# Kernel optimization log

Hardware: AMD Instinct MI355X
Metric: run time of the kernel (lower is better)

## Reference

```python
import jax, jax.numpy as jnp
import numpy as np
import math

N_QUBITS = 6
N_LAYERS = 3
OUT_DIM = 8
B = 131072
F = 24


def _gate_rx(a):
    # RX(a) = [[cos(a/2), -i sin(a/2)], [-i sin(a/2), cos(a/2)]]; a: scalar or [B]
    c = jnp.cos(a / 2).astype(jnp.complex64)
    s = (-1j * jnp.sin(a / 2)).astype(jnp.complex64)
    return jnp.stack([jnp.stack([c, s], -1), jnp.stack([s, c], -1)], -2)


def _gate_ry(a):
    c = jnp.cos(a / 2).astype(jnp.complex64)
    s = jnp.sin(a / 2).astype(jnp.complex64)
    return jnp.stack([jnp.stack([c, -s], -1), jnp.stack([s, c], -1)], -2)


def _gate_rz(a):
    # RZ(a) = diag(e^{-ia/2}, e^{ia/2})
    e = jnp.exp(-0.5j * a.astype(jnp.complex64))
    z = jnp.zeros_like(e)
    return jnp.stack([jnp.stack([e, z], -1), jnp.stack([z, jnp.conj(e)], -1)], -2)


def _apply_1q(state, gate, q, batched):
    # state: [B] + [2]*N_QUBITS ; gate: [2,2] or [B,2,2]
    s = jnp.moveaxis(state, 1 + q, 1)
    if batched:
        out = jnp.einsum('bij,bj...->bi...', gate, s)
    else:
        out = jnp.einsum('ij,bj...->bi...', gate, s)
    return jnp.moveaxis(out, 1, 1 + q)


def _apply_cnot(state, c, t):
    # flip target where control bit == 1
    cax = 1 + c
    s0 = jnp.take(state, 0, axis=cax)
    s1 = jnp.take(state, 1, axis=cax)
    tax = 1 + t if t < c else t  # control axis removed
    s1 = jnp.flip(s1, axis=tax)
    return jnp.stack([s0, s1], axis=cax)


def _circuit(x, theta):
    Bn = x.shape[0]
    # pooling branch of forward: chunks of size ceil(F/n_qubits)=4, mean each
    x_packed = x.reshape(Bn, N_QUBITS, F // N_QUBITS).mean(-1)
    angles = jnp.clip(x_packed, -6.0, 6.0) / 6.0 * math.pi  # [B, n_qubits]

    state = jnp.zeros((Bn,) + (2,) * N_QUBITS, dtype=jnp.complex64)
    state = state.at[(slice(None),) + (0,) * N_QUBITS].set(1.0)

    # angle encoding: RX(a_q), RZ(0.5*a_q) per qubit (batched gates)
    for q in range(N_QUBITS):
        state = _apply_1q(state, _gate_rx(angles[:, q]), q, batched=True)
        state = _apply_1q(state, _gate_rz(0.5 * angles[:, q]), q, batched=True)

    for l in range(N_LAYERS):
        for q in range(N_QUBITS - 1):
            state = _apply_cnot(state, q, q + 1)
        state = _apply_cnot(state, N_QUBITS - 1, 0)
        for q in range(N_QUBITS):
            state = _apply_1q(state, _gate_rx(theta[l, q, 0]), q, batched=False)
            state = _apply_1q(state, _gate_ry(theta[l, q, 1]), q, batched=False)
            state = _apply_1q(state, _gate_rz(theta[l, q, 2]), q, batched=False)

    probs = jnp.abs(state) ** 2  # real
    meas = []
    for k in range(OUT_DIM):
        q = k % N_QUBITS
        if k % 2 == 0:  # PauliZ
            pq = jnp.sum(probs, axis=tuple(a for a in range(1, N_QUBITS + 1) if a != 1 + q))
            meas.append(pq[:, 0] - pq[:, 1])
        else:  # PauliX: Re <psi| X_q |psi>
            flipped = jnp.flip(state, axis=1 + q)
            meas.append(jnp.real(jnp.sum(jnp.conj(state) * flipped, axis=tuple(range(1, N_QUBITS + 1)))))
    return jnp.stack(meas, axis=1).astype(jnp.float32)  # [B, out_dim]


def setup_inputs() -> dict:
    key = jax.random.key(0)
    k1, k2 = jax.random.split(key)
    x = jax.random.normal(k1, (B, F), dtype=jnp.float32)
    theta = jax.random.normal(k2, (N_LAYERS, N_QUBITS, 3), dtype=jnp.float32) * 0.1
    return {"x": x, "theta": theta}


def reference(x, theta):
    return _circuit(x, theta)
```

## Files before the change

kernel.cpp:

```cpp
#include <hip/hip_runtime.h>
#include <math.h>


typedef _Float16 half8v __attribute__((ext_vector_type(8)));
typedef _Float16 half4v __attribute__((ext_vector_type(4)));
typedef float    float4v __attribute__((ext_vector_type(4)));

__device__ __forceinline__ float2 pk_cmul(float2 g, float2 a) {
    float2 t;
    asm("v_pk_mul_f32 %0, %1, %2 op_sel:[0,0] op_sel_hi:[0,1]"
        : "=v"(t) : "v"(g), "v"(a));
    asm("v_pk_fma_f32 %0, %1, %2, %0 op_sel:[1,1,0] op_sel_hi:[1,0,1] neg_lo:[1,0,0]"
        : "+v"(t) : "v"(g), "v"(a));
    return t;
}
__device__ __forceinline__ float2 pk_cmac(float2 acc, float2 g, float2 a) {
    asm("v_pk_fma_f32 %0, %1, %2, %0 op_sel:[0,0,0] op_sel_hi:[0,1,1]"
        : "+v"(acc) : "v"(g), "v"(a));
    asm("v_pk_fma_f32 %0, %1, %2, %0 op_sel:[1,1,0] op_sel_hi:[1,0,1] neg_lo:[1,0,0]"
        : "+v"(acc) : "v"(g), "v"(a));
    return acc;
}

__device__ __forceinline__ float xpair(float v) {
    return __int_as_float(__builtin_amdgcn_mov_dpp(__float_as_int(v), 0xB1, 0xF, 0xF, true));
}
__device__ __forceinline__ float2 xpair2(float2 v) {
    return make_float2(xpair(v.x), xpair(v.y));
}

template<int M>
__device__ __forceinline__ void apply1q(float2* st, float2 g00, float2 g01,
                                        float2 g10, float2 g11) {
#pragma unroll
    for (int j = 0; j < 32; ++j) {
        if (j & M) continue;
        float2 a = st[j], b = st[j + M];
        float2 na = pk_cmul(g00, a); na = pk_cmac(na, g01, b);
        float2 nb = pk_cmul(g10, a); nb = pk_cmac(nb, g11, b);
        st[j] = na; st[j + M] = nb;
    }
}

template<int MC, int MT>
__device__ __forceinline__ void cnot(float2* st) {
#pragma unroll
    for (int j = 0; j < 32; ++j) {
        if ((j & MC) && !(j & MT)) {
            float2 tmp = st[j]; st[j] = st[j + MT]; st[j + MT] = tmp;
        }
    }
}

struct cf { float r, i; };
__device__ __forceinline__ cf scmul(cf a, cf b) {
    return { fmaf(a.r, b.r, -a.i * b.i), fmaf(a.r, b.i, a.i * b.r) };
}

__device__ __forceinline__ int rpos(int row, int k) {
    return ((((row >> 4) * 4 + (k >> 5)) * 4 + ((k >> 3) & 3)) * 16 + (row & 15)) * 8 + (k & 7);
}

__global__ __launch_bounds__(128) void ubuild_kernel(
    const float* __restrict__ theta, float* __restrict__ Rw) {
    __shared__ float2 gs[18 * 4];
    const int t = threadIdx.x;
    if (t < 18) {
        const float* th = theta + t * 3;
        float sx, cx, sy, cy, sz, cz;
        __sincosf(0.5f * th[0], &sx, &cx);
        __sincosf(0.5f * th[1], &sy, &cy);
        __sincosf(0.5f * th[2], &sz, &cz);
        cf m00 = {  cy * cx,  sy * sx };
        cf m01 = { -sy * cx, -cy * sx };
        cf m10 = {  sy * cx, -cy * sx };
        cf m11 = {  cy * cx, -sy * sx };
        cf e0 = { cz, -sz }, e1 = { cz, sz };
        cf g00 = scmul(e0, m00), g01 = scmul(e0, m01);
        cf g10 = scmul(e1, m10), g11 = scmul(e1, m11);
        float2* o = gs + t * 4;
        o[0] = make_float2(g00.r, g00.i);
        o[1] = make_float2(g01.r, g01.i);
        o[2] = make_float2(g10.r, g10.i);
        o[3] = make_float2(g11.r, g11.i);
    }
    __syncthreads();

    const int c  = t >> 1;
    const bool pb = (t & 1) != 0;

    const int  target = c & 31;
    const bool mine   = ((c >> 5) == (pb ? 1 : 0));
    float2 st[32];
#pragma unroll
    for (int j = 0; j < 32; ++j)
        st[j] = make_float2((mine && j == target) ? 1.f : 0.f, 0.f);

#pragma unroll 1
    for (int l = 0; l < 3; ++l) {
#pragma unroll
        for (int j = 0; j < 16; ++j) {
            float2 lo = st[j], hi = st[j + 16];
            st[j].x      = pb ? hi.x : lo.x;  st[j].y      = pb ? hi.y : lo.y;
            st[j + 16].x = pb ? lo.x : hi.x;  st[j + 16].y = pb ? lo.y : hi.y;
        }
        cnot<16, 8>(st);
        cnot< 8, 4>(st);
        cnot< 4, 2>(st);
        cnot< 2, 1>(st);
#pragma unroll
        for (int j = 1; j < 32; j += 2) st[j] = xpair2(st[j]);

        const float2* g = gs + l * 24;
        {
            float2 q00 = g[0], q01 = g[1], q10 = g[2], q11 = g[3];
            float2 gm, go;
            gm.x = pb ? q11.x : q00.x;  gm.y = pb ? q11.y : q00.y;
            go.x = pb ? q10.x : q01.x;  go.y = pb ? q10.y : q01.y;
#pragma unroll
            for (int j = 0; j < 32; ++j) {
                float2 other = xpair2(st[j]);
                float2 nv = pk_cmul(gm, st[j]);
                st[j] = pk_cmac(nv, go, other);
            }
        }
        apply1q<16>(st, g[ 4], g[ 5], g[ 6], g[ 7]);
        apply1q< 8>(st, g[ 8], g[ 9], g[10], g[11]);
        apply1q< 4>(st, g[12], g[13], g[14], g[15]);
        apply1q< 2>(st, g[16], g[17], g[18], g[19]);
        apply1q< 1>(st, g[20], g[21], g[22], g[23]);
    }

#pragma unroll
    for (int j = 0; j < 32; ++j) {
        const int a = (pb ? 32 : 0) + j;
        const float re = st[j].x, im = st[j].y;
        Rw[rpos(a,      c)]      =  re;
        Rw[rpos(a,      c + 64)] = -im;
        Rw[rpos(a + 64, c)]      =  im;
        Rw[rpos(a + 64, c + 64)] =  re;
    }
}

__global__ __launch_bounds__(512) void qsim2_kernel(
    const float* __restrict__ x, const float* __restrict__ Rg,
    float* __restrict__ out) {
    __shared__ __align__(16) _Float16 A[2][16384];
    const int t = threadIdx.x;

#pragma unroll
    for (int ii = 0; ii < 8; ++ii) {
        const int idx = ii * 2048 + t * 4;
        float4 v = *reinterpret_cast<const float4*>(Rg + idx);
        half4v hi, lo;
        hi[0] = (_Float16)v.x; lo[0] = (_Float16)(v.x - (float)hi[0]);
        hi[1] = (_Float16)v.y; lo[1] = (_Float16)(v.y - (float)hi[1]);
        hi[2] = (_Float16)v.z; lo[2] = (_Float16)(v.z - (float)hi[2]);
        hi[3] = (_Float16)v.w; lo[3] = (_Float16)(v.w - (float)hi[3]);
        *reinterpret_cast<half4v*>(&A[0][idx]) = hi;
        *reinterpret_cast<half4v*>(&A[1][idx]) = lo;
    }
    __syncthreads();

    const int l = t & 63, w = t >> 6;
    const int e16 = l & 15, h = l >> 4;
    const int elem = (blockIdx.x * 8 + w) * 16 + e16;

    const float4* xv = reinterpret_cast<const float4*>(x + (size_t)elem * 24);
    float2 v0[6], v1[6];
#pragma unroll
    for (int q = 0; q < 6; ++q) {
        float4 xq = xv[q];
        float m = (xq.x + xq.y + xq.z + xq.w) * 0.25f;
        m = fminf(fmaxf(m, -6.0f), 6.0f);
        float a = m * 0.52359877559829887308f;
        float s2, c2, s4, c4;
        __sincosf(0.50f * a, &s2, &c2);
        __sincosf(0.25f * a, &s4, &c4);
        v0[q] = make_float2(c4 * c2, -s4 * c2);
        v1[q] = make_float2(s4 * s2, -c4 * s2);
    }
    float2 u01[4], T[8];
    u01[0] = pk_cmul(v0[4], v0[5]);
    u01[1] = pk_cmul(v0[4], v1[5]);
    u01[2] = pk_cmul(v1[4], v0[5]);
    u01[3] = pk_cmul(v1[4], v1[5]);
#pragma unroll
    for (int j = 0; j < 8; ++j)
        T[j] = pk_cmul((j & 4) ? v1[3] : v0[3], u01[j & 3]);
    float2 Q  = pk_cmul((h & 2) ? v1[1] : v0[1], (h & 1) ? v1[2] : v0[2]);
    float2 P1 = pk_cmul(v0[0], Q);
    float2 P2 = pk_cmul(v1[0], Q);

    half8v bhi[4], blo[4];
#pragma unroll
    for (int j = 0; j < 8; ++j) {
        float2 a1 = pk_cmul(P1, T[j]);
        float2 a2 = pk_cmul(P2, T[j]);
        { _Float16 hh = (_Float16)a1.x; bhi[0][j] = hh; blo[0][j] = (_Float16)(a1.x - (float)hh); }
        { _Float16 hh = (_Float16)a2.x; bhi[1][j] = hh; blo[1][j] = (_Float16)(a2.x - (float)hh); }
        { _Float16 hh = (_Float16)a1.y; bhi[2][j] = hh; blo[2][j] = (_Float16)(a1.y - (float)hh); }
        { _Float16 hh = (_Float16)a2.y; bhi[3][j] = hh; blo[3][j] = (_Float16)(a2.y - (float)hh); }
    }

    float4v acc[8];
#pragma unroll
    for (int m = 0; m < 8; ++m) acc[m] = (float4v){0.f, 0.f, 0.f, 0.f};
#pragma unroll
    for (int m = 0; m < 8; ++m) {
#pragma unroll
        for (int s = 0; s < 4; ++s) {
            const int fo = ((m * 4 + s) * 64 + l) * 8;
            half8v ah = *reinterpret_cast<const half8v*>(&A[0][fo]);
            half8v al = *reinterpret_cast<const half8v*>(&A[1][fo]);
            acc[m] = __builtin_amdgcn_mfma_f32_16x16x32_f16(ah, bhi[s], acc[m], 0, 0, 0);
            acc[m] = __builtin_amdgcn_mfma_f32_16x16x32_f16(ah, blo[s], acc[m], 0, 0, 0);
            acc[m] = __builtin_amdgcn_mfma_f32_16x16x32_f16(al, bhi[s], acc[m], 0, 0, 0);
        }
    }

    float z0 = 0.f, z2 = 0.f, z4 = 0.f, x1 = 0.f, x3 = 0.f, x5 = 0.f;
#pragma unroll
    for (int m = 0; m < 4; ++m)
#pragma unroll
        for (int r = 0; r < 4; ++r) {
            float re = acc[m][r], im = acc[m + 4][r];
            float p = fmaf(re, re, im * im);
            z0 += (m < 2) ? p : -p;
            z2 += p;
            z4 += (r < 2) ? p : -p;
        }
#pragma unroll
    for (int m = 0; m < 4; m += 2)
#pragma unroll
        for (int r = 0; r < 4; ++r)
            x1 += fmaf(acc[m][r], acc[m + 1][r], acc[m + 4][r] * acc[m + 5][r]);
#pragma unroll
    for (int m = 0; m < 4; ++m)
#pragma unroll
        for (int r = 0; r < 4; r += 2)
            x5 += fmaf(acc[m][r], acc[m][r + 1], acc[m + 4][r] * acc[m + 4][r + 1]);
#pragma unroll
    for (int m = 0; m < 8; ++m)
#pragma unroll
        for (int r = 0; r < 4; ++r) {
            float v = acc[m][r];
            x3 = fmaf(v, __shfl_xor(v, 16, 64), x3);
        }
    if (h >= 2) z2 = -z2;

#pragma unroll
    for (int d = 16; d <= 32; d <<= 1) {
        z0 += __shfl_xor(z0, d, 64);
        z2 += __shfl_xor(z2, d, 64);
        z4 += __shfl_xor(z4, d, 64);
        x1 += __shfl_xor(x1, d, 64);
        x3 += __shfl_xor(x3, d, 64);
        x5 += __shfl_xor(x5, d, 64);
    }
    x1 *= 2.f; x5 *= 2.f;

    if (h == 0)
        *reinterpret_cast<float4*>(out + (size_t)elem * 8) = make_float4(z0, x1, z2, x3);
    else if (h == 1)
        *reinterpret_cast<float4*>(out + (size_t)elem * 8 + 4) = make_float4(z4, x5, z0, x1);
}

extern "C" void kernel_launch(void* const* d_in, const int* in_sizes, int n_in,
                              void* d_out, int out_size, void* d_ws, size_t ws_size,
                              hipStream_t stream) {
    const float* x     = (const float*)d_in[0];
    const float* theta = (const float*)d_in[1];
    float* out = (float*)d_out;
    float* R   = (float*)d_ws;
    const int B = in_sizes[0] / 24;
    ubuild_kernel<<<dim3(1), dim3(128), 0, stream>>>(theta, R);
    qsim2_kernel<<<dim3(B / 128), dim3(512), 0, stream>>>(x, R, out);
}
```

Baseline: 86.78 us.

## Pre-split unitary to fp16 hi/lo in build kernel and DMA it into LDS

The build kernel now permutes the rows of the unitary and writes it to the workspace already split into fp16 hi/lo halves. The main kernel loads that data straight into LDS with global_load_lds instead of converting it per block, and overlaps the load with the angle-encoding arithmetic before a single barrier. It also derives the half-angle sincos from the quarter-angle one, packs conversions with cvt_pkrtz, and uses the row permutation to replace the cross-lane shuffle in the x3 reduction with register-local products. Occupancy is hinted with launch_bounds(512,2), and the pkrtz rounding mode changes the hi/lo split slightly.

```diff
diff --git a/kernel.cpp b/kernel.cpp
--- a/kernel.cpp
+++ b/kernel.cpp
@@ -3,7 +3,7 @@
 
 
 typedef _Float16 half8v __attribute__((ext_vector_type(8)));
-typedef _Float16 half4v __attribute__((ext_vector_type(4)));
+typedef __fp16   fp16x2 __attribute__((ext_vector_type(2)));
 typedef float    float4v __attribute__((ext_vector_type(4)));
 
 __device__ __forceinline__ float2 pk_cmul(float2 g, float2 a) {
@@ -61,9 +61,15 @@
     return ((((row >> 4) * 4 + (k >> 5)) * 4 + ((k >> 3) & 3)) * 16 + (row & 15)) * 8 + (k & 7);
 }
 
+__device__ __forceinline__ int permrow(int a) {
+    return (((a >> 4) & 1) << 5) | (((a >> 2) & 1) << 4) | (((a >> 5) & 1) << 3)
+         | (((a >> 3) & 1) << 2) | ((a & 1) << 1) | ((a >> 1) & 1);
+}
+
 __global__ __launch_bounds__(128) void ubuild_kernel(
     const float* __restrict__ theta, float* __restrict__ Rw) {
     __shared__ float2 gs[18 * 4];
+    __shared__ float Rls[16384];
     const int t = threadIdx.x;
     if (t < 18) {
         const float* th = theta + t * 3;
@@ -133,34 +139,52 @@
 
 #pragma unroll
     for (int j = 0; j < 32; ++j) {
-        const int a = (pb ? 32 : 0) + j;
+        const int a  = (pb ? 32 : 0) + j;
+        const int pr = permrow(a);
         const float re = st[j].x, im = st[j].y;
-        Rw[rpos(a,      c)]      =  re;
-        Rw[rpos(a,      c + 64)] = -im;
-        Rw[rpos(a + 64, c)]      =  im;
-        Rw[rpos(a + 64, c + 64)] =  re;
-    }
-}
-
-__global__ __launch_bounds__(512) void qsim2_kernel(
+        Rls[rpos(pr,      c)]      =  re;
+        Rls[rpos(pr,      c + 64)] = -im;
+        Rls[rpos(pr + 64, c)]      =  im;
+        Rls[rpos(pr + 64, c + 64)] =  re;
+    }
+    __syncthreads();
+
+    unsigned short* hiw = (unsigned short*)Rw;
+    unsigned short* low = hiw + 16384;
+    const int base = t * 128;
+#pragma unroll 1
+    for (int n = 0; n < 128; n += 8) {
+        half8v hv, lv;
+#pragma unroll
+        for (int u = 0; u < 8; ++u) {
+            float xx = Rls[base + n + u];
+            _Float16 hh = (_Float16)xx;
+            hv[u] = hh;
+            lv[u] = (_Float16)(xx - (float)hh);
+        }
+        *reinterpret_cast<half8v*>(hiw + base + n) = hv;
+        *reinterpret_cast<half8v*>(low + base + n) = lv;
+    }
+}
+
+__global__ __launch_bounds__(512, 2) void qsim2_kernel(
     const float* __restrict__ x, const float* __restrict__ Rg,
     float* __restrict__ out) {
-    __shared__ __align__(16) _Float16 A[2][16384];
+    __shared__ __align__(16) unsigned short Abuf[32768];
     const int t = threadIdx.x;
 
-#pragma unroll
-    for (int ii = 0; ii < 8; ++ii) {
-        const int idx = ii * 2048 + t * 4;
-        float4 v = *reinterpret_cast<const float4*>(Rg + idx);
-        half4v hi, lo;
-        hi[0] = (_Float16)v.x; lo[0] = (_Float16)(v.x - (float)hi[0]);
-        hi[1] = (_Float16)v.y; lo[1] = (_Float16)(v.y - (float)hi[1]);
-        hi[2] = (_Float16)v.z; lo[2] = (_Float16)(v.z - (float)hi[2]);
-        hi[3] = (_Float16)v.w; lo[3] = (_Float16)(v.w - (float)hi[3]);
-        *reinterpret_cast<half4v*>(&A[0][idx]) = hi;
-        *reinterpret_cast<half4v*>(&A[1][idx]) = lo;
-    }
-    __syncthreads();
+    {
+        const float4* g4 = reinterpret_cast<const float4*>(Rg);
+        const int wv = t >> 6;
+#pragma unroll
+        for (int ii = 0; ii < 8; ++ii) {
+            const float4* gp = g4 + ii * 512 + t;
+            unsigned short* lp = Abuf + ii * 4096 + wv * 512;
+            __builtin_amdgcn_global_load_lds(
+                (const __attribute__((address_space(1))) unsigned int*)gp,
+                (__attribute__((address_space(3))) unsigned int*)lp, 16, 0, 0);
+        }
+    }
 
     const int l = t & 63, w = t >> 6;
     const int e16 = l & 15, h = l >> 4;
@@ -174,9 +198,10 @@
         float m = (xq.x + xq.y + xq.z + xq.w) * 0.25f;
         m = fminf(fmaxf(m, -6.0f), 6.0f);
         float a = m * 0.52359877559829887308f;
-        float s2, c2, s4, c4;
-        __sincosf(0.50f * a, &s2, &c2);
+        float s4, c4;
         __sincosf(0.25f * a, &s4, &c4);
+        float s2 = 2.f * s4 * c4;
+        float c2 = fmaf(-2.f * s4, s4, 1.f);
         v0[q] = make_float2(c4 * c2, -s4 * c2);
         v1[q] = make_float2(s4 * s2, -c4 * s2);
     }
@@ -194,14 +219,25 @@
 
     half8v bhi[4], blo[4];
 #pragma unroll
-    for (int j = 0; j < 8; ++j) {
-        float2 a1 = pk_cmul(P1, T[j]);
-        float2 a2 = pk_cmul(P2, T[j]);
-        { _Float16 hh = (_Float16)a1.x; bhi[0][j] = hh; blo[0][j] = (_Float16)(a1.x - (float)hh); }
-        { _Float16 hh = (_Float16)a2.x; bhi[1][j] = hh; blo[1][j] = (_Float16)(a2.x - (float)hh); }
-        { _Float16 hh = (_Float16)a1.y; bhi[2][j] = hh; blo[2][j] = (_Float16)(a1.y - (float)hh); }
-        { _Float16 hh = (_Float16)a2.y; bhi[3][j] = hh; blo[3][j] = (_Float16)(a2.y - (float)hh); }
-    }
+    for (int j = 0; j < 8; j += 2) {
+        float2 a1a = pk_cmul(P1, T[j]), a1b = pk_cmul(P1, T[j + 1]);
+        float2 a2a = pk_cmul(P2, T[j]), a2b = pk_cmul(P2, T[j + 1]);
+#define SPLIT(S, va, vb)                                                      \
+        {                                                                     \
+            fp16x2 hp = __builtin_amdgcn_cvt_pkrtz(va, vb);                   \
+            fp16x2 lp = __builtin_amdgcn_cvt_pkrtz(va - (float)hp[0],         \
+                                                   vb - (float)hp[1]);        \
+            bhi[S][j] = (_Float16)hp[0]; bhi[S][j + 1] = (_Float16)hp[1];     \
+            blo[S][j] = (_Float16)lp[0]; blo[S][j + 1] = (_Float16)lp[1];     \
+        }
+        SPLIT(0, a1a.x, a1b.x)
+        SPLIT(1, a2a.x, a2b.x)
+        SPLIT(2, a1a.y, a1b.y)
+        SPLIT(3, a2a.y, a2b.y)
+#undef SPLIT
+    }
+
+    __syncthreads();
 
     float4v acc[8];
 #pragma unroll
@@ -211,43 +247,42 @@
 #pragma unroll
         for (int s = 0; s < 4; ++s) {
             const int fo = ((m * 4 + s) * 64 + l) * 8;
-            half8v ah = *reinterpret_cast<const half8v*>(&A[0][fo]);
-            half8v al = *reinterpret_cast<const half8v*>(&A[1][fo]);
+            half8v ah = *reinterpret_cast<const half8v*>(&Abuf[fo]);
+            half8v al = *reinterpret_cast<const half8v*>(&Abuf[16384 + fo]);
             acc[m] = __builtin_amdgcn_mfma_f32_16x16x32_f16(ah, bhi[s], acc[m], 0, 0, 0);
             acc[m] = __builtin_amdgcn_mfma_f32_16x16x32_f16(ah, blo[s], acc[m], 0, 0, 0);
             acc[m] = __builtin_amdgcn_mfma_f32_16x16x32_f16(al, bhi[s], acc[m], 0, 0, 0);
         }
     }
 
-    float z0 = 0.f, z2 = 0.f, z4 = 0.f, x1 = 0.f, x3 = 0.f, x5 = 0.f;
+    float tot = 0.f, z4 = 0.f, x1 = 0.f, x3 = 0.f, x5 = 0.f;
 #pragma unroll
     for (int m = 0; m < 4; ++m)
 #pragma unroll
         for (int r = 0; r < 4; ++r) {
             float re = acc[m][r], im = acc[m + 4][r];
             float p = fmaf(re, re, im * im);
-            z0 += (m < 2) ? p : -p;
-            z2 += p;
-            z4 += (r < 2) ? p : -p;
-        }
+            tot += p;
+            z4 += (r & 1) ? -p : p;
+        }
+#pragma unroll
+    for (int m = 0; m < 2; ++m)
+#pragma unroll
+        for (int r = 0; r < 4; ++r)
+            x1 += fmaf(acc[m][r], acc[m + 2][r], acc[m + 4][r] * acc[m + 6][r]);
 #pragma unroll
     for (int m = 0; m < 4; m += 2)
 #pragma unroll
         for (int r = 0; r < 4; ++r)
-            x1 += fmaf(acc[m][r], acc[m + 1][r], acc[m + 4][r] * acc[m + 5][r]);
+            x3 += fmaf(acc[m][r], acc[m + 1][r], acc[m + 4][r] * acc[m + 5][r]);
 #pragma unroll
     for (int m = 0; m < 4; ++m)
 #pragma unroll
-        for (int r = 0; r < 4; r += 2)
-            x5 += fmaf(acc[m][r], acc[m][r + 1], acc[m + 4][r] * acc[m + 4][r + 1]);
-#pragma unroll
-    for (int m = 0; m < 8; ++m)
-#pragma unroll
-        for (int r = 0; r < 4; ++r) {
-            float v = acc[m][r];
-            x3 = fmaf(v, __shfl_xor(v, 16, 64), x3);
-        }
-    if (h >= 2) z2 = -z2;
+        for (int r = 0; r < 2; ++r)
+            x5 += fmaf(acc[m][r], acc[m][r + 2], acc[m + 4][r] * acc[m + 4][r + 2]);
+
+    float z0 = (h & 2) ? -tot : tot;
+    float z2 = (h & 1) ? -tot : tot;
 
 #pragma unroll
     for (int d = 16; d <= 32; d <<= 1) {
@@ -258,7 +293,7 @@
         x3 += __shfl_xor(x3, d, 64);
         x5 += __shfl_xor(x5, d, 64);
     }
-    x1 *= 2.f; x5 *= 2.f;
+    x1 *= 2.f; x3 *= 2.f; x5 *= 2.f;
 
     if (h == 0)
         *reinterpret_cast<float4*>(out + (size_t)elem * 8) = make_float4(z0, x1, z2, x3);
```

Measured after the change: 85.18 us. Within noise of the previous version (-1.8%).
